# Optimization experiments

Measured on AMD Instinct MI355X. Metric: run time of the kernel, lower is better.

## Reference

```python
import jax, jax.numpy as jnp
import numpy as np

NUM_HEADS = 4
KERNEL = 4
EPS = 1e-6


def _causal_conv1d(x, w, b):
    # x: (B,S,D), w: (D,1,K) depthwise, b: (D,)
    xc = x.transpose(0, 2, 1)  # (B,D,S)
    y = jax.lax.conv_general_dilated(
        xc, w, window_strides=(1,), padding=[(w.shape[-1] - 1, 0)],
        feature_group_count=xc.shape[1])
    return (y + b[None, :, None]).transpose(0, 2, 1)  # (B,S,D)


def _headwise(x, w):
    # x: (B,S,D), w: (NH, DH_out, DH_in) block-diagonal linear, no bias
    B, S, D = x.shape
    nh, dout, din = w.shape
    xh = x.reshape(B, S, nh, din)
    return jnp.einsum('bshd,hod->bsho', xh, w).reshape(B, S, nh * dout)


def _slstm_scan(gates, R, b):
    # gates: (B,S,4,NH,DH) ordered [i,f,z,o]; R: (NH,DH,4*DH); b: (4,NH,DH)
    B, S, _, nh, dh = gates.shape
    gseq = gates.transpose(1, 0, 2, 3, 4)  # (S,B,4,NH,DH)
    zero = jnp.zeros((B, nh, dh), gates.dtype)
    init = (zero, zero, zero, zero)  # h, c, n, m

    def step(carry, g):
        h, c, n, m = carry
        rec = jnp.einsum('bhd,hdk->bhk', h, R)
        rec = rec.reshape(B, nh, 4, dh).transpose(0, 2, 1, 3)  # (B,4,NH,DH)
        raw = g + rec + b[None]
        iraw, fraw, zraw, oraw = raw[:, 0], raw[:, 1], raw[:, 2], raw[:, 3]
        logfplusm = m + jax.nn.log_sigmoid(fraw)
        m_new = jnp.maximum(iraw, logfplusm)  # stabilizer
        ig = jnp.exp(iraw - m_new)
        fg = jnp.exp(logfplusm - m_new)
        c_new = fg * c + ig * jnp.tanh(zraw)
        n_new = fg * n + ig
        h_new = jax.nn.sigmoid(oraw) * c_new / n_new
        return (h_new, c_new, n_new, m_new), h_new

    _, ys = jax.lax.scan(step, init, gseq)  # ys: (S,B,NH,DH)
    return ys.transpose(1, 2, 0, 3)  # (B,NH,S,DH)


def _multihead_layernorm(y, scale, bias):
    # y: (B,NH,S,DH); normalize over DH per head
    mu = y.mean(-1, keepdims=True)
    var = y.var(-1, keepdims=True)
    yn = (y - mu) * jax.lax.rsqrt(var + EPS)
    nh, dh = y.shape[1], y.shape[3]
    return yn * scale.reshape(1, nh, 1, dh) + bias.reshape(1, nh, 1, dh)


def setup_inputs() -> dict:
    key = jax.random.key(0)
    ks = jax.random.split(key, 12)
    B, S, D = 4, 2048, 1024
    nh, dh = NUM_HEADS, D // NUM_HEADS
    sd_conv = 1.0 / np.sqrt(KERNEL)
    sd_head = 1.0 / np.sqrt(dh)
    return {
        'x': jax.random.normal(ks[0], (B, S, D), jnp.float32),
        'conv_w': jax.random.normal(ks[1], (D, 1, KERNEL), jnp.float32) * sd_conv,
        'conv_b': jnp.zeros((D,), jnp.float32),
        'w_i': jax.random.normal(ks[2], (nh, dh, dh), jnp.float32) * sd_head,
        'w_f': jax.random.normal(ks[3], (nh, dh, dh), jnp.float32) * sd_head,
        'w_z': jax.random.normal(ks[4], (nh, dh, dh), jnp.float32) * sd_head,
        'w_o': jax.random.normal(ks[5], (nh, dh, dh), jnp.float32) * sd_head,
        'rec_kernel': jax.random.normal(ks[6], (nh, dh, 4 * dh), jnp.float32) * sd_head,
        'cell_bias': jnp.zeros((4, nh, dh), jnp.float32),
        'gn_scale': jnp.ones((D,), jnp.float32),
        'gn_bias': jnp.zeros((D,), jnp.float32),
    }


def reference(x, conv_w, conv_b, w_i, w_f, w_z, w_o, rec_kernel, cell_bias, gn_scale, gn_bias):
    B, S, D = x.shape
    dh = D // NUM_HEADS
    x_conv = jax.nn.swish(_causal_conv1d(x, conv_w, conv_b))
    i = _headwise(x_conv, w_i)
    f = _headwise(x_conv, w_f)
    z = _headwise(x, w_z)
    o = _headwise(x, w_o)
    # concat order [i,f,z,o]; reshape to (B,S,4,NH,DH)
    gates = jnp.stack([i, f, z, o], axis=2).reshape(B, S, 4, NUM_HEADS, dh)
    y = _slstm_scan(gates, rec_kernel, cell_bias)  # (B,NH,S,DH)
    out = _multihead_layernorm(y, gn_scale, gn_bias)
    return out.transpose(0, 2, 1, 3).reshape(B, S, D)
```

## Files before the change

kernel.cpp:

```cpp
#include <hip/hip_runtime.h>
#include <hip/hip_bf16.h>

#define NH 4
#define DH 256
#define DMODEL 1024
#define BB 4
#define SS 2048

typedef __attribute__((ext_vector_type(4))) float f32x4;
typedef __attribute__((ext_vector_type(8))) short bf16x8;
typedef __attribute__((ext_vector_type(4))) int i32x4;

__device__ __forceinline__ int dot4i8(int acc, int a, int b) {
#if __has_builtin(__builtin_amdgcn_sdot4)
    return __builtin_amdgcn_sdot4(a, b, acc, false);
#else
#pragma unroll
    for (int i = 0; i < 4; ++i) {
        int av = (a << (24 - 8 * i)) >> 24;
        int bv = (b << (24 - 8 * i)) >> 24;
        acc += av * bv;
    }
    return acc;
#endif
}

__global__ void k_conv(const float* __restrict__ x, const float* __restrict__ cw,
                       const float* __restrict__ cb, float* __restrict__ xc) {
    int bs = blockIdx.x;
    int s = bs & (SS - 1);
    const float* xrow = x + (size_t)bs * DMODEL;
#pragma unroll
    for (int dd = 0; dd < 4; ++dd) {
        int d = threadIdx.x + dd * 256;
        float w0 = cw[d * 4 + 0], w1 = cw[d * 4 + 1], w2 = cw[d * 4 + 2], w3 = cw[d * 4 + 3];
        float acc = cb[d] + w3 * xrow[d];
        if (s >= 1) acc += w2 * xrow[d - DMODEL];
        if (s >= 2) acc += w1 * xrow[d - 2 * DMODEL];
        if (s >= 3) acc += w0 * xrow[d - 3 * DMODEL];
        float sig = 1.f / (1.f + __expf(-acc));
        xc[(size_t)bs * DMODEL + d] = acc * sig;
    }
}

__global__ void k_gemm(const float* __restrict__ x, const float* __restrict__ xc,
                       const float* __restrict__ wi, const float* __restrict__ wf,
                       const float* __restrict__ wz, const float* __restrict__ wo,
                       float* __restrict__ gates) {
    int h = blockIdx.z >> 1, pair = blockIdx.z & 1;
    const float* A = pair ? x : xc;
    int n0 = blockIdx.y * 64;
    const float* W = (n0 < 256) ? (pair ? wz : wi) : (pair ? wo : wf);
    int nl = n0 & 255;
    int m0 = blockIdx.x * 64;

    __shared__ __align__(16) __hip_bfloat16 Al[64][72];
    __shared__ __align__(16) __hip_bfloat16 Bl[64][72];

    int tid = threadIdx.x;
    int lane = tid & 63, wv = tid >> 6;
    f32x4 acc[4] = {};

    for (int k0 = 0; k0 < 256; k0 += 64) {
        __syncthreads();
#pragma unroll
        for (int i = 0; i < 4; ++i) {
            int f4 = tid + i * 256;
            int r = f4 >> 4, c4 = (f4 & 15) * 4;
            const float* srcA = A + (size_t)(m0 + r) * DMODEL + h * DH + k0 + c4;
            float4 v = *(const float4*)srcA;
            Al[r][c4 + 0] = __float2bfloat16(v.x);
            Al[r][c4 + 1] = __float2bfloat16(v.y);
            Al[r][c4 + 2] = __float2bfloat16(v.z);
            Al[r][c4 + 3] = __float2bfloat16(v.w);
            const float* srcB = W + (size_t)(h * DH + nl + r) * DH + k0 + c4;
            float4 u = *(const float4*)srcB;
            Bl[r][c4 + 0] = __float2bfloat16(u.x);
            Bl[r][c4 + 1] = __float2bfloat16(u.y);
            Bl[r][c4 + 2] = __float2bfloat16(u.z);
            Bl[r][c4 + 3] = __float2bfloat16(u.w);
        }
        __syncthreads();
#pragma unroll
        for (int kk = 0; kk < 64; kk += 32) {
            bf16x8 a = *(const bf16x8*)&Al[wv * 16 + (lane & 15)][kk + (lane >> 4) * 8];
#pragma unroll
            for (int nt = 0; nt < 4; ++nt) {
                bf16x8 bfr = *(const bf16x8*)&Bl[nt * 16 + (lane & 15)][kk + (lane >> 4) * 8];
                acc[nt] = __builtin_amdgcn_mfma_f32_16x16x32_bf16(a, bfr, acc[nt], 0, 0, 0);
            }
        }
    }
#pragma unroll
    for (int nt = 0; nt < 4; ++nt)
#pragma unroll
        for (int r = 0; r < 4; ++r) {
            int m = m0 + wv * 16 + (lane >> 4) * 4 + r;
            int n = n0 + nt * 16 + (lane & 15);
            int b = m >> 11, s = m & (SS - 1);
            int g = pair * 2 + (n >> 8), d = n & 255;
            gates[((((size_t)(b * NH + h)) * SS + s) * 4 + g) * DH + d] = acc[nt][r];
        }
}

__global__ void k_prep(const float* __restrict__ R, int* __restrict__ Wq,
                       float* __restrict__ scales) {
    int colid = blockIdx.x * 4 + (threadIdx.x >> 6);
    int lane = threadIdx.x & 63;
    int h = colid >> 10, k = colid & 1023;
    const float* base = R + (size_t)h * 256 * 1024 + k;
    float v[4];
    float mx = 0.f;
#pragma unroll
    for (int i = 0; i < 4; ++i) {
        v[i] = base[(size_t)(lane * 4 + i) * 1024];
        mx = fmaxf(mx, fabsf(v[i]));
    }
    for (int off = 32; off; off >>= 1) mx = fmaxf(mx, __shfl_xor(mx, off));
    mx = fmaxf(mx, 1e-30f);
    float scale = mx * (1.f / 127.f);
    float inv = 127.f / mx;
    int pk = 0;
#pragma unroll
    for (int i = 0; i < 4; ++i) {
        int q = (int)rintf(v[i] * inv);
        q = max(-127, min(127, q));
        pk |= (q & 255) << (8 * i);
    }
    Wq[(h * 64 + lane) * 1024 + k] = pk;
    if (lane == 0) scales[h * 1024 + k] = scale;
}

__launch_bounds__(1024, 4)
__global__ void k_scan(const float* __restrict__ gates, const int* __restrict__ Wq,
                       const float* __restrict__ scales, const float* __restrict__ bias,
                       float* __restrict__ y) {
    int bh = blockIdx.x;
    int h = bh & 3;
    int t = threadIdx.x;

    __shared__ __align__(16) signed char hq[256];
    __shared__ float rec[1024];

    int w[64];
#pragma unroll
    for (int j = 0; j < 64; ++j) w[j] = Wq[(h * 64 + j) * 1024 + t];
    float colmul = scales[h * 1024 + t] * (1.f / 127.f);

    float c = 0.f, n = 0.f, mstate = 0.f;
    float bi = 0.f, bf_ = 0.f, bz = 0.f, bo = 0.f;
    int d = t;
    if (t < 256) {
        bi = bias[(0 * NH + h) * DH + d];
        bf_ = bias[(1 * NH + h) * DH + d];
        bz = bias[(2 * NH + h) * DH + d];
        bo = bias[(3 * NH + h) * DH + d];
    }
    if (t < 16) ((i32x4*)hq)[t] = (i32x4){0, 0, 0, 0};
    const float* gbase = gates + (size_t)bh * SS * 1024;
    float* ybase = y + (size_t)bh * SS * DH;
    __syncthreads();

    for (int s = 0; s < SS; ++s) {
        float gi = 0.f, gf = 0.f, gz = 0.f, go = 0.f;
        if (t < 256) {
            const float* gp = gbase + (size_t)s * 1024 + d;
            gi = gp[0]; gf = gp[256]; gz = gp[512]; go = gp[768];
        }
        int acc = 0;
#pragma unroll
        for (int g4 = 0; g4 < 4; ++g4) {
            i32x4 h0 = ((const i32x4*)hq)[g4 * 4 + 0];
            i32x4 h1 = ((const i32x4*)hq)[g4 * 4 + 1];
            i32x4 h2 = ((const i32x4*)hq)[g4 * 4 + 2];
            i32x4 h3 = ((const i32x4*)hq)[g4 * 4 + 3];
            acc = dot4i8(acc, w[g4 * 16 + 0], h0.x);
            acc = dot4i8(acc, w[g4 * 16 + 1], h0.y);
            acc = dot4i8(acc, w[g4 * 16 + 2], h0.z);
            acc = dot4i8(acc, w[g4 * 16 + 3], h0.w);
            acc = dot4i8(acc, w[g4 * 16 + 4], h1.x);
            acc = dot4i8(acc, w[g4 * 16 + 5], h1.y);
            acc = dot4i8(acc, w[g4 * 16 + 6], h1.z);
            acc = dot4i8(acc, w[g4 * 16 + 7], h1.w);
            acc = dot4i8(acc, w[g4 * 16 + 8], h2.x);
            acc = dot4i8(acc, w[g4 * 16 + 9], h2.y);
            acc = dot4i8(acc, w[g4 * 16 + 10], h2.z);
            acc = dot4i8(acc, w[g4 * 16 + 11], h2.w);
            acc = dot4i8(acc, w[g4 * 16 + 12], h3.x);
            acc = dot4i8(acc, w[g4 * 16 + 13], h3.y);
            acc = dot4i8(acc, w[g4 * 16 + 14], h3.z);
            acc = dot4i8(acc, w[g4 * 16 + 15], h3.w);
        }
        rec[t] = (float)acc * colmul;
        __syncthreads();
        if (t < 256) {
            float ri = rec[d], rf = rec[256 + d], rz = rec[512 + d], ro = rec[768 + d];
            float rawi = gi + ri + bi;
            float rawf = gf + rf + bf_;
            float rawz = gz + rz + bz;
            float rawo = go + ro + bo;
            float lsf = fminf(rawf, 0.f) - __logf(1.f + __expf(-fabsf(rawf)));
            float lfm = mstate + lsf;
            float mn = fmaxf(rawi, lfm);
            float ig = __expf(rawi - mn);
            float fg = __expf(lfm - mn);
            float az = fabsf(rawz);
            float e2 = __expf(-2.f * az);
            float th = (1.f - e2) / (1.f + e2);
            th = rawz < 0.f ? -th : th;
            c = fg * c + ig * th;
            n = fg * n + ig;
            mstate = mn;
            float so = 1.f / (1.f + __expf(-rawo));
            float hv = so * c / n;
            ybase[(size_t)s * DH + d] = hv;
            int q = (int)rintf(hv * 127.f);
            hq[d] = (signed char)q;
        }
        __syncthreads();
    }
}

__global__ void k_ln(const float* __restrict__ y, const float* __restrict__ gsc,
                     const float* __restrict__ gbi, float* __restrict__ out) {
    int bid = blockIdx.x;
    int s = bid & (SS - 1);
    int bh = bid >> 11;
    int b = bh >> 2, h = bh & 3;
    int d = threadIdx.x;
    float v = y[(size_t)bid * DH + d];
    float s1 = v, s2 = v * v;
    for (int off = 32; off; off >>= 1) {
        s1 += __shfl_xor(s1, off);
        s2 += __shfl_xor(s2, off);
    }
    __shared__ float a1[4], a2[4];
    int wv = threadIdx.x >> 6, ln = threadIdx.x & 63;
    if (ln == 0) { a1[wv] = s1; a2[wv] = s2; }
    __syncthreads();
    s1 = a1[0] + a1[1] + a1[2] + a1[3];
    s2 = a2[0] + a2[1] + a2[2] + a2[3];
    float mu = s1 * (1.f / 256.f);
    float var = s2 * (1.f / 256.f) - mu * mu;
    float rs = rsqrtf(var + 1e-6f);
    float o = (v - mu) * rs * gsc[h * DH + d] + gbi[h * DH + d];
    out[((size_t)(b * SS + s)) * DMODEL + h * DH + d] = o;
}

extern "C" void kernel_launch(void* const* d_in, const int* in_sizes, int n_in,
                              void* d_out, int out_size, void* d_ws, size_t ws_size,
                              hipStream_t stream) {
    (void)in_sizes; (void)n_in; (void)out_size; (void)ws_size;
    const float* x = (const float*)d_in[0];
    const float* cw = (const float*)d_in[1];
    const float* cb = (const float*)d_in[2];
    const float* wi = (const float*)d_in[3];
    const float* wf = (const float*)d_in[4];
    const float* wz = (const float*)d_in[5];
    const float* wo = (const float*)d_in[6];
    const float* R = (const float*)d_in[7];
    const float* cbias = (const float*)d_in[8];
    const float* gsc = (const float*)d_in[9];
    const float* gbi = (const float*)d_in[10];
    float* out = (float*)d_out;

    char* ws = (char*)d_ws;
    float* xc = (float*)ws;
    float* gates = (float*)(ws + 33554432ull);
    float* yb = (float*)(ws + 167772160ull);
    int* Wq = (int*)(ws + 201326592ull);
    float* scales = (float*)(ws + 202375168ull);

    k_prep<<<1024, 256, 0, stream>>>(R, Wq, scales);
    k_conv<<<BB * SS, 256, 0, stream>>>(x, cw, cb, xc);
    k_gemm<<<dim3(128, 8, 8), 256, 0, stream>>>(x, xc, wi, wf, wz, wo, gates);
    k_scan<<<16, 1024, 0, stream>>>(gates, Wq, scales, cbias, yb);
    k_ln<<<BB * SS * NH, 256, 0, stream>>>(yb, gsc, gbi, out);
}
```

Measured before the change: 2.107 ms.

## Compute sLSTM recurrent matvec with int8 MFMA and prefetch gates two steps ahead

Replaces the per-thread sdot4 loop in the recurrent scan with int8 MFMA (16x16x64) instructions. Each of 8 waves holds a slice of the quantized recurrent weights in registers as MFMA B fragments, and the quantized h vector is fed as the A operand; only row 0 of each output tile is used. The block shrinks to 512 threads, gate results are stored interleaved as int so one i32x4 load gathers all four gates, and gate inputs are prefetched two timesteps ahead via a 2-way unrolled loop. The goal is to cut the latency of the serial per-step matvec. The cost is that most MFMA lanes are wasted, and a custom barrier with an lgkmcnt wait is added.

```diff
diff --git a/kernel.cpp b/kernel.cpp
--- a/kernel.cpp
+++ b/kernel.cpp
@@ -11,18 +11,10 @@
 typedef __attribute__((ext_vector_type(8))) short bf16x8;
 typedef __attribute__((ext_vector_type(4))) int i32x4;
 
-__device__ __forceinline__ int dot4i8(int acc, int a, int b) {
-#if __has_builtin(__builtin_amdgcn_sdot4)
-    return __builtin_amdgcn_sdot4(a, b, acc, false);
-#else
-#pragma unroll
-    for (int i = 0; i < 4; ++i) {
-        int av = (a << (24 - 8 * i)) >> 24;
-        int bv = (b << (24 - 8 * i)) >> 24;
-        acc += av * bv;
-    }
-    return acc;
-#endif
+__device__ __forceinline__ void wg_barrier() {
+    asm volatile("s_waitcnt lgkmcnt(0)" ::: "memory");
+    __builtin_amdgcn_s_barrier();
+    __builtin_amdgcn_sched_barrier(0);
 }
 
 __global__ void k_conv(const float* __restrict__ x, const float* __restrict__ cw,
@@ -131,94 +123,128 @@
     if (lane == 0) scales[h * 1024 + k] = scale;
 }
 
-__launch_bounds__(1024, 4)
+__launch_bounds__(512, 2)
 __global__ void k_scan(const float* __restrict__ gates, const int* __restrict__ Wq,
                        const float* __restrict__ scales, const float* __restrict__ bias,
                        float* __restrict__ y) {
     int bh = blockIdx.x;
     int h = bh & 3;
     int t = threadIdx.x;
+    int lane = t & 63;
+    int wv = t >> 6;
+    int kg = lane >> 4;
+    int cl = lane & 15;
 
     __shared__ __align__(16) signed char hq[256];
-    __shared__ float rec[1024];
-
-    int w[64];
-#pragma unroll
-    for (int j = 0; j < 64; ++j) w[j] = Wq[(h * 64 + j) * 1024 + t];
-    float colmul = scales[h * 1024 + t] * (1.f / 127.f);
-
-    float c = 0.f, n = 0.f, mstate = 0.f;
-    float bi = 0.f, bf_ = 0.f, bz = 0.f, bo = 0.f;
+    __shared__ __align__(16) int rec_i[DH * 4];
+
+    i32x4 bfr[8][4];
+#pragma unroll
+    for (int tt = 0; tt < 8; ++tt) {
+        int col = (wv * 8 + tt) * 16 + cl;
+#pragma unroll
+        for (int c = 0; c < 4; ++c)
+#pragma unroll
+            for (int j4 = 0; j4 < 4; ++j4)
+                bfr[tt][c][j4] = Wq[(h * 64 + c * 16 + kg * 4 + j4) * 1024 + col];
+    }
+
+    int raddr[8];
+#pragma unroll
+    for (int tt = 0; tt < 8; ++tt) {
+        int col = (wv * 8 + tt) * 16 + lane;
+        raddr[tt] = ((col & 255) * 4 + (col >> 8)) * 4;
+    }
+
+    i32x4 acc[8];
+#pragma unroll
+    for (int tt = 0; tt < 8; ++tt) acc[tt] = (i32x4){0, 0, 0, 0};
+
     int d = t;
+    float cm0 = 0, cm1 = 0, cm2 = 0, cm3 = 0, bi = 0, bf_ = 0, bz = 0, bo = 0;
+    const float* gbase = gates + (size_t)bh * SS * 1024;
+    float* ybase = y + (size_t)bh * SS * DH;
     if (t < 256) {
+        cm0 = scales[h * 1024 + d] * (1.f / 127.f);
+        cm1 = scales[h * 1024 + 256 + d] * (1.f / 127.f);
+        cm2 = scales[h * 1024 + 512 + d] * (1.f / 127.f);
+        cm3 = scales[h * 1024 + 768 + d] * (1.f / 127.f);
         bi = bias[(0 * NH + h) * DH + d];
         bf_ = bias[(1 * NH + h) * DH + d];
         bz = bias[(2 * NH + h) * DH + d];
         bo = bias[(3 * NH + h) * DH + d];
     }
+    float c_ = 0.f, n_ = 0.f, mstate = 0.f;
+
     if (t < 16) ((i32x4*)hq)[t] = (i32x4){0, 0, 0, 0};
-    const float* gbase = gates + (size_t)bh * SS * 1024;
-    float* ybase = y + (size_t)bh * SS * DH;
     __syncthreads();
 
-    for (int s = 0; s < SS; ++s) {
-        float gi = 0.f, gf = 0.f, gz = 0.f, go = 0.f;
-        if (t < 256) {
-            const float* gp = gbase + (size_t)s * 1024 + d;
-            gi = gp[0]; gf = gp[256]; gz = gp[512]; go = gp[768];
-        }
-        int acc = 0;
-#pragma unroll
-        for (int g4 = 0; g4 < 4; ++g4) {
-            i32x4 h0 = ((const i32x4*)hq)[g4 * 4 + 0];
-            i32x4 h1 = ((const i32x4*)hq)[g4 * 4 + 1];
-            i32x4 h2 = ((const i32x4*)hq)[g4 * 4 + 2];
-            i32x4 h3 = ((const i32x4*)hq)[g4 * 4 + 3];
-            acc = dot4i8(acc, w[g4 * 16 + 0], h0.x);
-            acc = dot4i8(acc, w[g4 * 16 + 1], h0.y);
-            acc = dot4i8(acc, w[g4 * 16 + 2], h0.z);
-            acc = dot4i8(acc, w[g4 * 16 + 3], h0.w);
-            acc = dot4i8(acc, w[g4 * 16 + 4], h1.x);
-            acc = dot4i8(acc, w[g4 * 16 + 5], h1.y);
-            acc = dot4i8(acc, w[g4 * 16 + 6], h1.z);
-            acc = dot4i8(acc, w[g4 * 16 + 7], h1.w);
-            acc = dot4i8(acc, w[g4 * 16 + 8], h2.x);
-            acc = dot4i8(acc, w[g4 * 16 + 9], h2.y);
-            acc = dot4i8(acc, w[g4 * 16 + 10], h2.z);
-            acc = dot4i8(acc, w[g4 * 16 + 11], h2.w);
-            acc = dot4i8(acc, w[g4 * 16 + 12], h3.x);
-            acc = dot4i8(acc, w[g4 * 16 + 13], h3.y);
-            acc = dot4i8(acc, w[g4 * 16 + 14], h3.z);
-            acc = dot4i8(acc, w[g4 * 16 + 15], h3.w);
-        }
-        rec[t] = (float)acc * colmul;
-        __syncthreads();
-        if (t < 256) {
-            float ri = rec[d], rf = rec[256 + d], rz = rec[512 + d], ro = rec[768 + d];
-            float rawi = gi + ri + bi;
-            float rawf = gf + rf + bf_;
-            float rawz = gz + rz + bz;
-            float rawo = go + ro + bo;
-            float lsf = fminf(rawf, 0.f) - __logf(1.f + __expf(-fabsf(rawf)));
-            float lfm = mstate + lsf;
-            float mn = fmaxf(rawi, lfm);
-            float ig = __expf(rawi - mn);
-            float fg = __expf(lfm - mn);
-            float az = fabsf(rawz);
-            float e2 = __expf(-2.f * az);
-            float th = (1.f - e2) / (1.f + e2);
-            th = rawz < 0.f ? -th : th;
-            c = fg * c + ig * th;
-            n = fg * n + ig;
-            mstate = mn;
-            float so = 1.f / (1.f + __expf(-rawo));
-            float hv = so * c / n;
-            ybase[(size_t)s * DH + d] = hv;
-            int q = (int)rintf(hv * 127.f);
-            hq[d] = (signed char)q;
-        }
-        __syncthreads();
-    }
+    float gA0 = 0, gA1 = 0, gA2 = 0, gA3 = 0, gB0 = 0, gB1 = 0, gB2 = 0, gB3 = 0;
+    if (t < 256) {
+        gA0 = gbase[d]; gA1 = gbase[256 + d]; gA2 = gbase[512 + d]; gA3 = gbase[768 + d];
+        gB0 = gbase[1024 + d]; gB1 = gbase[1024 + 256 + d];
+        gB2 = gbase[1024 + 512 + d]; gB3 = gbase[1024 + 768 + d];
+    }
+
+    const i32x4* hp = (const i32x4*)hq;
+    const i32x4* rp = (const i32x4*)rec_i;
+
+#define SCAN_STEP(SCUR, G0, G1, G2, G3)                                        \
+    {                                                                          \
+        float p0 = 0, p1 = 0, p2 = 0, p3 = 0;                                  \
+        if (t < 256) {                                                         \
+            int sp = (SCUR) + 2 < SS ? (SCUR) + 2 : SS - 1;                    \
+            const float* gp = gbase + (size_t)sp * 1024 + d;                   \
+            p0 = gp[0]; p1 = gp[256]; p2 = gp[512]; p3 = gp[768];              \
+        }                                                                      \
+                     \
+        i32x4 a0 = hp[kg], a1 = hp[4 + kg], a2 = hp[8 + kg], a3 = hp[12 + kg]; \
+        _Pragma("unroll") for (int tt = 0; tt < 8; ++tt) acc[tt].x = 0;        \
+        _Pragma("unroll") for (int tt = 0; tt < 8; ++tt)                       \
+            acc[tt] = __builtin_amdgcn_mfma_i32_16x16x64_i8(a0, bfr[tt][0], acc[tt], 0, 0, 0); \
+        _Pragma("unroll") for (int tt = 0; tt < 8; ++tt)                       \
+            acc[tt] = __builtin_amdgcn_mfma_i32_16x16x64_i8(a1, bfr[tt][1], acc[tt], 0, 0, 0); \
+        _Pragma("unroll") for (int tt = 0; tt < 8; ++tt)                       \
+            acc[tt] = __builtin_amdgcn_mfma_i32_16x16x64_i8(a2, bfr[tt][2], acc[tt], 0, 0, 0); \
+        _Pragma("unroll") for (int tt = 0; tt < 8; ++tt)                       \
+            acc[tt] = __builtin_amdgcn_mfma_i32_16x16x64_i8(a3, bfr[tt][3], acc[tt], 0, 0, 0); \
+        if (lane < 16) {                                                       \
+            _Pragma("unroll") for (int tt = 0; tt < 8; ++tt)                   \
+                *(int*)((char*)rec_i + raddr[tt]) = acc[tt].x;                 \
+        }                                                                      \
+        wg_barrier();                                                          \
+        if (t < 256) {                                                         \
+            i32x4 r4 = rp[d];                                                  \
+            float rawi = (G0) + (float)r4.x * cm0 + bi;                        \
+            float rawf = (G1) + (float)r4.y * cm1 + bf_;                       \
+            float rawz = (G2) + (float)r4.z * cm2 + bz;                        \
+            float rawo = (G3) + (float)r4.w * cm3 + bo;                        \
+            float lsf = fminf(rawf, 0.f) - __logf(1.f + __expf(-fabsf(rawf))); \
+            float lfm = mstate + lsf;                                          \
+            float mn = fmaxf(rawi, lfm);                                       \
+            float ig = __expf(rawi - mn);                                      \
+            float fg = __expf(lfm - mn);                                       \
+            float az = fabsf(rawz);                                            \
+            float e2 = __expf(-2.f * az);                                      \
+            float th = (1.f - e2) / (1.f + e2);                                \
+            th = rawz < 0.f ? -th : th;                                        \
+            c_ = fg * c_ + ig * th;                                            \
+            n_ = fg * n_ + ig;                                                 \
+            mstate = mn;                                                       \
+            float so = 1.f / (1.f + __expf(-rawo));                            \
+            float hv = so * c_ / n_;                                           \
+            ybase[(size_t)(SCUR)*DH + d] = hv;                                 \
+            hq[d] = (signed char)(int)rintf(hv * 127.f);                       \
+        }                                                                      \
+        G0 = p0; G1 = p1; G2 = p2; G3 = p3;                                    \
+        wg_barrier();                                                          \
+    }
+
+    for (int s = 0; s < SS; s += 2) {
+        SCAN_STEP(s, gA0, gA1, gA2, gA3)
+        SCAN_STEP(s + 1, gB0, gB1, gB2, gB3)
+    }
+#undef SCAN_STEP
 }
 
 __global__ void k_ln(const float* __restrict__ y, const float* __restrict__ gsc,
@@ -274,6 +300,6 @@
     k_prep<<<1024, 256, 0, stream>>>(R, Wq, scales);
     k_conv<<<BB * SS, 256, 0, stream>>>(x, cw, cb, xc);
     k_gemm<<<dim3(128, 8, 8), 256, 0, stream>>>(x, xc, wi, wf, wz, wo, gates);
-    k_scan<<<16, 1024, 0, stream>>>(gates, Wq, scales, cbias, yb);
+    k_scan<<<16, 512, 0, stream>>>(gates, Wq, scales, cbias, yb);
     k_ln<<<BB * SS * NH, 256, 0, stream>>>(yb, gsc, gbi, out);
 }
```

Result: no change. 2.079 ms (-1.3%).
